# Kernel tuning notes

Measured on AMD Instinct MI355X. Metric: run time of the kernel, lower is better.

Reference implementation:

```python
import jax, jax.numpy as jnp
import numpy as np

B, T, C, H = 256, 256, 384, 64  # batch, seq (= block_size), n_embd, head_size


def setup_inputs() -> dict:
    key = jax.random.key(0)
    kx, kq, kk, kv = jax.random.split(key, 4)
    x = jax.random.normal(kx, (B, T, C), dtype=jnp.float32)
    # nn.Linear(n_embd, head_size, bias=False) weights, stored transposed so y = x @ W
    scale = 1.0 / np.sqrt(C)
    Wq = jax.random.normal(kq, (C, H), dtype=jnp.float32) * scale
    Wk = jax.random.normal(kk, (C, H), dtype=jnp.float32) * scale
    Wv = jax.random.normal(kv, (C, H), dtype=jnp.float32) * scale
    return {"x": x, "Wq": Wq, "Wk": Wk, "Wv": Wv}


def reference(x, Wq, Wk, Wv):
    # Single causal self-attention head. NOTE: source scales by C**-0.5 where
    # C = n_embd (not head_size) — preserved faithfully. Dropout in eval mode
    # (identity) for a deterministic reference.
    Bv, Tv, Cv = x.shape
    q = x @ Wq                                   # [B, T, H]
    k = x @ Wk                                   # [B, T, H]
    v = x @ Wv                                   # [B, T, H]
    wei = jnp.einsum('bth,bsh->bts', q, k) * (Cv ** -0.5)  # [B, T, T]
    causal = jnp.tril(jnp.ones((Tv, Tv), dtype=bool))      # tril[:T,:T]
    wei = jnp.where(causal[None, :, :], wei, -jnp.inf)
    wei = jax.nn.softmax(wei, axis=-1)
    out = jnp.einsum('bts,bsh->bth', wei, v)     # [B, T, H]
    return out
```

## Files before the change

### kernel.cpp

```cpp
#include <hip/hip_runtime.h>
#include <hip/hip_bf16.h>

typedef __attribute__((ext_vector_type(8))) short bf16x8;
typedef __attribute__((ext_vector_type(4))) float f32x4;

__device__ __forceinline__ unsigned short f2bf(float f) {
    union { float f; unsigned int u; } v; v.f = f;
    unsigned int u = v.u;
    unsigned int r = u + 0x7FFFu + ((u >> 16) & 1u);
    return (unsigned short)(r >> 16);
}

__device__ __forceinline__ unsigned int cvtpk(float lo, float hi) {
    unsigned int r;
    asm("v_cvt_pk_bf16_f32 %0, %1, %2" : "=v"(r) : "v"(lo), "v"(hi));
    return r;
}

__device__ __forceinline__ float frcp(float x) {
    float r;
    asm("v_rcp_f32 %0, %1" : "=v"(r) : "v"(x));
    return r;
}

#define GLDS16(gsrc, ldst)                                                          \
    __builtin_amdgcn_global_load_lds(                                               \
        (const __attribute__((address_space(1))) unsigned int*)(gsrc),              \
        (__attribute__((address_space(3))) unsigned int*)(ldst), 16, 0, 0)

__global__ __launch_bounds__(256) void wprep(const float* __restrict__ Wq,
                                             const float* __restrict__ Wk,
                                             const float* __restrict__ Wv,
                                             unsigned short* __restrict__ Wt2) {
    int idx = blockIdx.x * 256 + threadIdx.x;
    if (idx >= 73728) return;
    int w   = idx / 24576;
    int rem = idx % 24576;
    int n = rem / 384, k = rem % 384;
    const float* W = (w == 0) ? Wq : ((w == 1) ? Wk : Wv);
    int col = w * 64 + n;
    int c = k >> 5, r = k & 31;
    int rr = r & 15;
    int lg = rr >> 2;
    int e  = ((r < 16) ? 0 : 4) + (rr & 3);
    Wt2[(size_t)c * 6144 + lg * 1536 + col * 8 + e] = f2bf(W[k * 64 + n]);
}

#define QOFF  0
#define KOFF  36864
#define VTOFF 73728
#define POFF  107520

template<int NT>
__device__ __forceinline__ void attn_strip16(char* smem, char* Pw, float* __restrict__ ob,
                                             int r0, int lane) {
    const int l15 = lane & 15, lg = lane >> 4;
    const float scale = 0.05103103630798287f;

    bf16x8 aq[2];
#pragma unroll
    for (int kk = 0; kk < 2; ++kk)
        aq[kk] = *reinterpret_cast<const bf16x8*>(smem + QOFF + ((r0 + l15) * 72 + kk * 32 + lg * 8) * 2);

    f32x4 s[NT][4] = {};
#pragma unroll
    for (int jt = 0; jt < NT; ++jt)
#pragma unroll
        for (int kk = 0; kk < 2; ++kk) {
            bf16x8 bk[4];
#pragma unroll
            for (int n = 0; n < 4; ++n)
                bk[n] = *reinterpret_cast<const bf16x8*>(smem + KOFF + ((jt * 64 + n * 16 + l15) * 72 + kk * 32 + lg * 8) * 2);
#pragma unroll
            for (int n = 0; n < 4; ++n)
                s[jt][n] = __builtin_amdgcn_mfma_f32_16x16x32_bf16(aq[kk], bk[n], s[jt][n], 0, 0, 0);
        }

    float M[4];
#pragma unroll
    for (int j = 0; j < 4; ++j) M[j] = -1e30f;
#pragma unroll
    for (int jt = 0; jt < NT; ++jt)
#pragma unroll
        for (int n = 0; n < 4; ++n) {
            int colg = jt * 64 + n * 16 + l15;
#pragma unroll
            for (int j = 0; j < 4; ++j) {
                float v = s[jt][n][j] * scale;
                if (jt == NT - 1) {
                    int rowg = r0 + lg * 4 + j;
                    if (colg > rowg) v = -1e30f;
                }
                s[jt][n][j] = v;
                M[j] = fmaxf(M[j], v);
            }
        }
#pragma unroll
    for (int j = 0; j < 4; ++j) {
        float v = M[j];
        v = fmaxf(v, __shfl_xor(v, 1));
        v = fmaxf(v, __shfl_xor(v, 2));
        v = fmaxf(v, __shfl_xor(v, 4));
        v = fmaxf(v, __shfl_xor(v, 8));
        M[j] = v;
    }
    float L[4] = {};
#pragma unroll
    for (int jt = 0; jt < NT; ++jt)
#pragma unroll
        for (int n = 0; n < 4; ++n)
#pragma unroll
            for (int j = 0; j < 4; ++j) {
                float p = __expf(s[jt][n][j] - M[j]);
                s[jt][n][j] = p;
                L[j] += p;
            }
    float rL[4];
#pragma unroll
    for (int j = 0; j < 4; ++j) {
        float v = L[j];
        v += __shfl_xor(v, 1);
        v += __shfl_xor(v, 2);
        v += __shfl_xor(v, 4);
        v += __shfl_xor(v, 8);
        rL[j] = frcp(v);
    }
    f32x4 o[4] = {};
#pragma unroll
    for (int jt = 0; jt < NT; ++jt) {
#pragma unroll
        for (int n = 0; n < 4; ++n)
#pragma unroll
            for (int j = 0; j < 4; ++j)
                *reinterpret_cast<unsigned short*>(Pw + ((lg * 4 + j) * 72 + n * 16 + l15) * 2) = f2bf(s[jt][n][j]);
        asm volatile("s_waitcnt lgkmcnt(0)" ::: "memory");
#pragma unroll
        for (int kk = 0; kk < 2; ++kk) {
            bf16x8 ap, bv[4];
            ap = *reinterpret_cast<const bf16x8*>(Pw + (l15 * 72 + kk * 32 + lg * 8) * 2);
#pragma unroll
            for (int n = 0; n < 4; ++n)
                bv[n] = *reinterpret_cast<const bf16x8*>(smem + VTOFF + ((n * 16 + l15) * 264 + jt * 64 + kk * 32 + lg * 8) * 2);
#pragma unroll
            for (int n = 0; n < 4; ++n)
                o[n] = __builtin_amdgcn_mfma_f32_16x16x32_bf16(ap, bv[n], o[n], 0, 0, 0);
        }
    }
    float* tf = reinterpret_cast<float*>(Pw);
#pragma unroll
    for (int n = 0; n < 4; ++n)
#pragma unroll
        for (int j = 0; j < 4; ++j)
            tf[(lg * 4 + j) * 68 + n * 16 + l15] = o[n][j] * rL[j];
    asm volatile("s_waitcnt lgkmcnt(0)" ::: "memory");
#pragma unroll
    for (int i = 0; i < 4; ++i) {
        int row = i * 4 + lg;
        float4 vv = *reinterpret_cast<const float4*>(&tf[row * 68 + l15 * 4]);
        *reinterpret_cast<float4*>(ob + (size_t)(r0 + row) * 64 + l15 * 4) = vv;
    }
}

__global__ __launch_bounds__(512, 1) void fused(const float* __restrict__ x,
                                                const unsigned short* __restrict__ Wt2,
                                                float* __restrict__ out) {
    __shared__ __align__(16) char smem[147456];

    const int b = blockIdx.x;
    const int tid = threadIdx.x, lane = tid & 63, wid = tid >> 6;
    const int l15 = lane & 15, lg = lane >> 4;
    const float* xb = x + (size_t)b * 98304;
    float* ob = out + (size_t)b * 16384;

#pragma unroll
    for (int i = 0; i < 18; ++i) {
        int n = wid * 18 + i;
        GLDS16(Wt2 + (size_t)n * 512 + lane * 8, smem + n * 1024);
    }

    const float* xw = xb + (size_t)(wid * 32 + l15) * 384 + lg * 4;

    float4 p0[4], p1[4], p2[4], p3[4], p4[4];
#define XLOAD(P, C)                                                                 \
    P[0] = *reinterpret_cast<const float4*>(xw + (C) * 32);                         \
    P[1] = *reinterpret_cast<const float4*>(xw + (C) * 32 + 16);                    \
    P[2] = *reinterpret_cast<const float4*>(xw + 6144 + (C) * 32);                  \
    P[3] = *reinterpret_cast<const float4*>(xw + 6144 + (C) * 32 + 16);
    XLOAD(p0, 0)
    XLOAD(p1, 1)
    XLOAD(p2, 2)
    XLOAD(p3, 3)
    XLOAD(p4, 4)
    __builtin_amdgcn_sched_barrier(0);
    asm volatile("s_waitcnt vmcnt(20)" ::: "memory");
    __builtin_amdgcn_s_barrier();

    f32x4 acc[2][12] = {};

#define CHUNK(C, P, WAITN)                                                          \
    asm volatile("s_waitcnt vmcnt(" #WAITN ")" ::: "memory");                       \
    __builtin_amdgcn_sched_barrier(0);                                              \
    {                                                                               \
        union { unsigned int u[4]; bf16x8 v; } cv0, cv1;                            \
        cv0.u[0] = cvtpk(P[0].x, P[0].y); cv0.u[1] = cvtpk(P[0].z, P[0].w);         \
        cv0.u[2] = cvtpk(P[1].x, P[1].y); cv0.u[3] = cvtpk(P[1].z, P[1].w);         \
        cv1.u[0] = cvtpk(P[2].x, P[2].y); cv1.u[1] = cvtpk(P[2].z, P[2].w);         \
        cv1.u[2] = cvtpk(P[3].x, P[3].y); cv1.u[3] = cvtpk(P[3].z, P[3].w);         \
        bf16x8 a0 = cv0.v, a1 = cv1.v;                                              \
        if ((C) + 5 < 12) { XLOAD(P, (C) + 5) }                                     \
        __builtin_amdgcn_sched_barrier(0);                                          \
        const char* bs = smem + (C) * 12288 + lg * 3072 + l15 * 16;                 \
        _Pragma("unroll")                                                           \
        for (int n = 0; n < 12; ++n) {                                              \
            bf16x8 bf = *reinterpret_cast<const bf16x8*>(bs + n * 256);             \
            acc[0][n] = __builtin_amdgcn_mfma_f32_16x16x32_bf16(a0, bf, acc[0][n], 0, 0, 0); \
            acc[1][n] = __builtin_amdgcn_mfma_f32_16x16x32_bf16(a1, bf, acc[1][n], 0, 0, 0); \
        }                                                                           \
    }

    CHUNK(0,  p0, 16)
    CHUNK(1,  p1, 16)
    CHUNK(2,  p2, 16)
    CHUNK(3,  p3, 16)
    CHUNK(4,  p4, 16)
    CHUNK(5,  p0, 16)
    CHUNK(6,  p1, 16)
    CHUNK(7,  p2, 16)
    CHUNK(8,  p3, 12)
    CHUNK(9,  p4, 8)
    CHUNK(10, p0, 4)
    CHUNK(11, p1, 0)

    __syncthreads();

#pragma unroll
    for (int m = 0; m < 2; ++m) {
        const int t0 = wid * 32 + m * 16 + lg * 4;
#pragma unroll
        for (int n = 0; n < 4; ++n) {
            int col = n * 16 + l15;
#pragma unroll
            for (int j = 0; j < 4; ++j)
                *reinterpret_cast<unsigned short*>(smem + QOFF + ((t0 + j) * 72 + col) * 2) = f2bf(acc[m][n][j]);
        }
#pragma unroll
        for (int n = 4; n < 8; ++n) {
            int col = (n - 4) * 16 + l15;
#pragma unroll
            for (int j = 0; j < 4; ++j)
                *reinterpret_cast<unsigned short*>(smem + KOFF + ((t0 + j) * 72 + col) * 2) = f2bf(acc[m][n][j]);
        }
#pragma unroll
        for (int n = 8; n < 12; ++n) {
            int h = (n - 8) * 16 + l15;
            ushort4 h4;
            h4.x = f2bf(acc[m][n][0]); h4.y = f2bf(acc[m][n][1]);
            h4.z = f2bf(acc[m][n][2]); h4.w = f2bf(acc[m][n][3]);
            *reinterpret_cast<ushort4*>(smem + VTOFF + (h * 264 + t0) * 2) = h4;
        }
    }
    __syncthreads();

    char* Pw = smem + POFF + wid * 4608;
    if (wid < 4) {
        attn_strip16<1>(smem, Pw, ob, wid * 16, lane);
        attn_strip16<4>(smem, Pw, ob, (15 - wid) * 16, lane);
    } else {
        attn_strip16<2>(smem, Pw, ob, wid * 16, lane);
        attn_strip16<3>(smem, Pw, ob, (15 - wid) * 16, lane);
    }
}

extern "C" void kernel_launch(void* const* d_in, const int* in_sizes, int n_in,
                              void* d_out, int out_size, void* d_ws, size_t ws_size,
                              hipStream_t stream) {
    const float* x  = (const float*)d_in[0];
    const float* Wq = (const float*)d_in[1];
    const float* Wk = (const float*)d_in[2];
    const float* Wv = (const float*)d_in[3];
    float* out = (float*)d_out;

    unsigned short* Wt2 = (unsigned short*)d_ws;

    wprep<<<288, 256, 0, stream>>>(Wq, Wk, Wv, Wt2);
    fused<<<256, 512, 0, stream>>>(x, Wt2, out);
}
```

Before: 38.81 us.

## Software-pipeline LDS weight fragments and shorten global prefetch depth in projection

The QKV projection loop now preloads weight fragments from shared memory into registers as two half-sets, fetching the next chunk's first half while the current chunk's second half is computing, so LDS latency overlaps MFMA work. The x prefetch ring is cut from five register buffers to three, with the vmcnt waits adjusted to match. This frees registers to hold the B fragments. The cost is less global-load latency hiding, since fewer x loads are in flight at any time.

```diff
diff --git a/kernel.cpp b/kernel.cpp
--- a/kernel.cpp
+++ b/kernel.cpp
@@ -180,7 +180,7 @@
 
     const float* xw = xb + (size_t)(wid * 32 + l15) * 384 + lg * 4;
 
-    float4 p0[4], p1[4], p2[4], p3[4], p4[4];
+    float4 p0[4], p1[4], p2[4];
 #define XLOAD(P, C)                                                                 \
     P[0] = *reinterpret_cast<const float4*>(xw + (C) * 32);                         \
     P[1] = *reinterpret_cast<const float4*>(xw + (C) * 32 + 16);                    \
@@ -189,47 +189,66 @@
     XLOAD(p0, 0)
     XLOAD(p1, 1)
     XLOAD(p2, 2)
-    XLOAD(p3, 3)
-    XLOAD(p4, 4)
     __builtin_amdgcn_sched_barrier(0);
-    asm volatile("s_waitcnt vmcnt(20)" ::: "memory");
+    asm volatile("s_waitcnt vmcnt(12)" ::: "memory");
     __builtin_amdgcn_s_barrier();
 
+    bf16x8 bL[6], bH[6];
+    {
+        const char* bs0 = smem + lg * 3072 + l15 * 16;
+#pragma unroll
+        for (int i = 0; i < 6; ++i)
+            bL[i] = *reinterpret_cast<const bf16x8*>(bs0 + i * 256);
+    }
+
     f32x4 acc[2][12] = {};
 
 #define CHUNK(C, P, WAITN)                                                          \
-    asm volatile("s_waitcnt vmcnt(" #WAITN ")" ::: "memory");                       \
-    __builtin_amdgcn_sched_barrier(0);                                              \
     {                                                                               \
+        const char* bsc = smem + (C) * 12288 + lg * 3072 + l15 * 16;                \
+        _Pragma("unroll")                                                           \
+        for (int i = 0; i < 6; ++i)                                                 \
+            bH[i] = *reinterpret_cast<const bf16x8*>(bsc + (6 + i) * 256);          \
+        asm volatile("s_waitcnt vmcnt(" #WAITN ")" ::: "memory");                   \
+        __builtin_amdgcn_sched_barrier(0);                                          \
         union { unsigned int u[4]; bf16x8 v; } cv0, cv1;                            \
         cv0.u[0] = cvtpk(P[0].x, P[0].y); cv0.u[1] = cvtpk(P[0].z, P[0].w);         \
         cv0.u[2] = cvtpk(P[1].x, P[1].y); cv0.u[3] = cvtpk(P[1].z, P[1].w);         \
         cv1.u[0] = cvtpk(P[2].x, P[2].y); cv1.u[1] = cvtpk(P[2].z, P[2].w);         \
         cv1.u[2] = cvtpk(P[3].x, P[3].y); cv1.u[3] = cvtpk(P[3].z, P[3].w);         \
         bf16x8 a0 = cv0.v, a1 = cv1.v;                                              \
-        if ((C) + 5 < 12) { XLOAD(P, (C) + 5) }                                     \
+        if ((C) + 3 < 12) { XLOAD(P, (C) + 3) }                                     \
         __builtin_amdgcn_sched_barrier(0);                                          \
-        const char* bs = smem + (C) * 12288 + lg * 3072 + l15 * 16;                 \
         _Pragma("unroll")                                                           \
-        for (int n = 0; n < 12; ++n) {                                              \
-            bf16x8 bf = *reinterpret_cast<const bf16x8*>(bs + n * 256);             \
-            acc[0][n] = __builtin_amdgcn_mfma_f32_16x16x32_bf16(a0, bf, acc[0][n], 0, 0, 0); \
-            acc[1][n] = __builtin_amdgcn_mfma_f32_16x16x32_bf16(a1, bf, acc[1][n], 0, 0, 0); \
+        for (int n = 0; n < 6; ++n) {                                               \
+            acc[0][n] = __builtin_amdgcn_mfma_f32_16x16x32_bf16(a0, bL[n], acc[0][n], 0, 0, 0); \
+            acc[1][n] = __builtin_amdgcn_mfma_f32_16x16x32_bf16(a1, bL[n], acc[1][n], 0, 0, 0); \
         }                                                                           \
-    }
-
-    CHUNK(0,  p0, 16)
-    CHUNK(1,  p1, 16)
-    CHUNK(2,  p2, 16)
-    CHUNK(3,  p3, 16)
-    CHUNK(4,  p4, 16)
-    CHUNK(5,  p0, 16)
-    CHUNK(6,  p1, 16)
-    CHUNK(7,  p2, 16)
-    CHUNK(8,  p3, 12)
-    CHUNK(9,  p4, 8)
-    CHUNK(10, p0, 4)
-    CHUNK(11, p1, 0)
+        if ((C) < 11) {                                                             \
+            const char* bsn = smem + ((C) + 1) * 12288 + lg * 3072 + l15 * 16;      \
+            _Pragma("unroll")                                                       \
+            for (int i = 0; i < 6; ++i)                                             \
+                bL[i] = *reinterpret_cast<const bf16x8*>(bsn + i * 256);            \
+        }                                                                           \
+        _Pragma("unroll")                                                           \
+        for (int n = 0; n < 6; ++n) {                                               \
+            acc[0][6 + n] = __builtin_amdgcn_mfma_f32_16x16x32_bf16(a0, bH[n], acc[0][6 + n], 0, 0, 0); \
+            acc[1][6 + n] = __builtin_amdgcn_mfma_f32_16x16x32_bf16(a1, bH[n], acc[1][6 + n], 0, 0, 0); \
+        }                                                                           \
+    }
+
+    CHUNK(0,  p0, 8)
+    CHUNK(1,  p1, 8)
+    CHUNK(2,  p2, 8)
+    CHUNK(3,  p0, 8)
+    CHUNK(4,  p1, 8)
+    CHUNK(5,  p2, 8)
+    CHUNK(6,  p0, 8)
+    CHUNK(7,  p1, 8)
+    CHUNK(8,  p2, 8)
+    CHUNK(9,  p0, 8)
+    CHUNK(10, p1, 4)
+    CHUNK(11, p2, 0)
 
     __syncthreads();
 
```

Result: faster. 37.66 us (-3.0%).
